# Kernel optimization log

Hardware: AMD Instinct MI355X
Metric: run time of the kernel (lower is better)

The kernel has to match this reference:

```python
import jax, jax.numpy as jnp
import numpy as np

B, C, H, W = 4, 192, 56, 56


def setup_inputs() -> dict:
    key = jax.random.key(0)
    k1, k2, k3 = jax.random.split(key, 3)
    x = jax.random.normal(k1, (B, C, H, W), dtype=jnp.float32)
    conv_w = jax.random.normal(k2, (C, 2 * C), dtype=jnp.float32) * (1.0 / np.sqrt(2 * C))
    conv_b = jax.random.normal(k3, (C,), dtype=jnp.float32) * 0.01
    bn_gamma = jnp.ones((C,), dtype=jnp.float32)
    bn_beta = jnp.zeros((C,), dtype=jnp.float32)
    bn_mean = jnp.zeros((C,), dtype=jnp.float32)
    bn_var = jnp.ones((C,), dtype=jnp.float32)
    return {"x": x, "conv_w": conv_w, "conv_b": conv_b, "bn_gamma": bn_gamma,
            "bn_beta": bn_beta, "bn_mean": bn_mean, "bn_var": bn_var, "K": 4}


def reference(x, conv_w, conv_b, bn_gamma, bn_beta, bn_mean, bn_var, K):
    b, c, h, w = x.shape
    shifts_h = list(range(0, h, K))          # rolls along H
    shifts_w = list(range(K, w, K))          # rolls along W
    n = len(shifts_h) + len(shifts_w)
    scale = n ** (-0.5)
    # (B, n, C, H, W): all circularly shifted copies (static shift set)
    rolled = jnp.stack([jnp.roll(x, i, axis=2) for i in shifts_h] +
                       [jnp.roll(x, j, axis=3) for j in shifts_w], axis=1)
    # scores: tanh(scale * x * x_rolled), summed over channels -> (B, n, 1, H, W)
    scores = jnp.tanh(rolled * x[:, None] * scale).sum(axis=2, keepdims=True)
    weights = jax.nn.softmax(scores, axis=1)
    out = (rolled * weights).sum(axis=1)     # (B, C, H, W)
    cat = jnp.concatenate([x, out], axis=1)  # (B, 2C, H, W)
    # 1x1 conv as GEMM over channels
    y = jnp.einsum('bchw,oc->bohw', cat, conv_w) + conv_b[None, :, None, None]
    # BatchNorm2d in eval mode (running stats)
    eps = 1e-5
    inv = bn_gamma / jnp.sqrt(bn_var + eps)
    y = (y - bn_mean[None, :, None, None]) * inv[None, :, None, None] + bn_beta[None, :, None, None]
    return jax.nn.gelu(y, approximate=False)
```

## Files before the change

### kernel.cpp

```cpp
#include <hip/hip_runtime.h>
#include <hip/hip_bf16.h>
#include <math.h>

#define BB 4
#define CC 192
#define HH 56
#define WW 56
#define HWW 3136

typedef __attribute__((ext_vector_type(8))) short short8;
typedef __attribute__((ext_vector_type(4))) float f32x4;

__device__ __forceinline__ unsigned short f2b(float f) {
    __hip_bfloat16 h = __float2bfloat16(f);
    return __builtin_bit_cast(unsigned short, h);
}
__device__ __forceinline__ float b2f(unsigned short u) {
    unsigned int x = ((unsigned int)u) << 16;
    return __builtin_bit_cast(float, x);
}

__global__ __launch_bounds__(256) void k_pre(const float* __restrict__ x,
                                             const float* __restrict__ cw,
                                             unsigned short* __restrict__ xth,
                                             unsigned short* __restrict__ xtl,
                                             unsigned short* __restrict__ cwh,
                                             unsigned short* __restrict__ cwl) {
    int tid = threadIdx.x, bid = blockIdx.x;
    if (bid < 2352) {
        __shared__ float tile[32][33];
        int b = bid / 588, rem = bid % 588;
        int by = rem / 98, bx = rem % 98;
        int tx = tid & 31, ty = tid >> 5;
        int p0 = bx * 32, c0 = by * 32;
#pragma unroll
        for (int i = 0; i < 4; i++) {
            int c = c0 + ty + 8 * i;
            tile[ty + 8 * i][tx] = x[(b * CC + c) * HWW + p0 + tx];
        }
        __syncthreads();
#pragma unroll
        for (int i = 0; i < 4; i++) {
            int p = p0 + ty + 8 * i;
            float v = tile[tx][ty + 8 * i];
            unsigned short hi = f2b(v);
            size_t o = (size_t)(b * HWW + p) * CC + c0 + tx;
            xth[o] = hi;
            xtl[o] = f2b(v - b2f(hi));
        }
    } else {
        int i = (bid - 2352) * 256 + tid;
        if (i < 384 * 192) {
            int n = i / 192, k = i % 192;
            float v = (n < 192) ? cw[n * 384 + k] : cw[(n - 192) * 384 + 192 + k];
            unsigned short hi = f2b(v);
            cwh[i] = hi;
            cwl[i] = f2b(v - b2f(hi));
        }
    }
}

__global__ __launch_bounds__(256) void k_mid(const unsigned short* __restrict__ xth,
                                             const unsigned short* __restrict__ xtl,
                                             const unsigned short* __restrict__ cwh,
                                             const unsigned short* __restrict__ cwl,
                                             float* __restrict__ sp,
                                             float* __restrict__ u,
                                             float* __restrict__ z) {
    __shared__ __align__(16) char smem[36864];
    int tid = threadIdx.x, bid = blockIdx.x;

    if (bid < 1792) {
        float* Xs = (float*)smem;
        const float K2 = 0.38490017945975050f;
        bool isH = bid < 896;
        int lid = isH ? bid : bid - 896;
        int half = lid & 1;
        int rp = (lid >> 1) & 1;
        int cb2 = lid >> 2;
        int b = cb2 / 56, l0 = cb2 % 56;
        int r0 = rp * 2;

        const unsigned short* srch = xth + (size_t)(b * HWW) * CC + half * 96;
        const unsigned short* srcl = xtl + (size_t)(b * HWW) * CC + half * 96;
        for (int idx = tid; idx < 28 * 12; idx += 256) {
            int t2 = idx / 12, cq = idx % 12;
            int pi = (r0 + t2 / 14) + 4 * (t2 % 14);
            int pix = isH ? (pi * WW + l0) : (l0 * WW + pi);
            short8 h8 = *(const short8*)(srch + (size_t)pix * CC + cq * 8);
            short8 l8 = *(const short8*)(srcl + (size_t)pix * CC + cq * 8);
            float o[8];
#pragma unroll
            for (int e = 0; e < 8; e++)
                o[e] = b2f((unsigned short)h8[e]) + b2f((unsigned short)l8[e]);
            *(float4*)&Xs[t2 * 100 + cq * 8] = *(float4*)&o[0];
            *(float4*)&Xs[t2 * 100 + cq * 8 + 4] = *(float4*)&o[4];
        }
        __syncthreads();

        int perCls = isH ? 105 : 91;
        if (tid < 2 * perCls) {
            int cls = tid / perCls, p = tid % perCls;
            int a, bb;
            if (isH) {
                a = (int)((sqrtf((float)(8 * p + 1)) - 1.0f) * 0.5f);
                bb = p - (a * (a + 1)) / 2;
            } else {
                int ap = (int)((sqrtf((float)(8 * p + 1)) - 1.0f) * 0.5f);
                bb = p - (ap * (ap + 1)) / 2;
                a = ap + 1;
            }
            const float* pA = &Xs[(cls * 14 + a) * 100];
            const float* pB = &Xs[(cls * 14 + bb) * 100];
            float s0 = 0.f, s1 = 0.f, s2 = 0.f, s3 = 0.f;
#pragma unroll
            for (int q = 0; q < 24; q++) {
                float4 av = *(const float4*)(pA + q * 4);
                float4 bv = *(const float4*)(pB + q * 4);
                s0 += __builtin_amdgcn_rcpf(__expf(av.x * bv.x * K2) + 1.0f);
                s1 += __builtin_amdgcn_rcpf(__expf(av.y * bv.y * K2) + 1.0f);
                s2 += __builtin_amdgcn_rcpf(__expf(av.z * bv.z * K2) + 1.0f);
                s3 += __builtin_amdgcn_rcpf(__expf(av.w * bv.w * K2) + 1.0f);
            }
            float s = 96.0f - 2.0f * (s0 + s1 + s2 + s3);
            int r = r0 + cls;
            size_t base = (size_t)(half * BB + b) * HWW;
            if (isH) {
                int i1 = a - bb;
                int h1 = r + 4 * a, h2 = r + 4 * bb;
                sp[(base + h1 * WW + l0) * 32 + i1] = s;
                if (a != bb) sp[(base + h2 * WW + l0) * 32 + (14 - i1)] = s;
            } else {
                int d = a - bb;
                int w1 = r + 4 * a, w2 = r + 4 * bb;
                sp[(base + l0 * WW + w1) * 32 + 14 + (d - 1)] = s;
                sp[(base + l0 * WW + w2) * 32 + 14 + (13 - d)] = s;
            }
        }
        return;
    }

    {
        unsigned short* Ah = (unsigned short*)smem;
        unsigned short* Al = Ah + 64 * 72;
        unsigned short* Bh = Ah + 2 * 64 * 72;
        unsigned short* Bl = Ah + 3 * 64 * 72;
        float* Ds = (float*)smem;
        int vb = bid - 1792;
        int bm = (vb % 196) * 64, bn = (vb / 196) * 64;
        int lane = tid & 63, wv = tid >> 6;

        f32x4 acc[4] = {{0,0,0,0},{0,0,0,0},{0,0,0,0},{0,0,0,0}};

        for (int kc = 0; kc < 3; kc++) {
#pragma unroll
            for (int r2 = 0; r2 < 2; r2++) {
                int idx = tid + r2 * 256;
                int m = idx >> 3, kq = idx & 7;
                size_t ao = (size_t)(bm + m) * CC + kc * 64 + kq * 8;
                *(short8*)&Ah[m * 72 + kq * 8] = *(const short8*)(xth + ao);
                *(short8*)&Al[m * 72 + kq * 8] = *(const short8*)(xtl + ao);
                size_t bo = (size_t)(bn + m) * 192 + kc * 64 + kq * 8;
                *(short8*)&Bh[m * 72 + kq * 8] = *(const short8*)(cwh + bo);
                *(short8*)&Bl[m * 72 + kq * 8] = *(const short8*)(cwl + bo);
            }
            __syncthreads();
            int n0 = wv * 16;
            int k8 = lane >> 4;
            int col = lane & 15;
#pragma unroll
            for (int ks = 0; ks < 64; ks += 32) {
                int koff = ks + k8 * 8;
                short8 bfh = *(const short8*)&Bh[(n0 + col) * 72 + koff];
                short8 bfl = *(const short8*)&Bl[(n0 + col) * 72 + koff];
#pragma unroll
                for (int fm = 0; fm < 4; fm++) {
                    short8 afh = *(const short8*)&Ah[(fm * 16 + col) * 72 + koff];
                    short8 afl = *(const short8*)&Al[(fm * 16 + col) * 72 + koff];
                    acc[fm] = __builtin_amdgcn_mfma_f32_16x16x32_bf16(afh, bfh, acc[fm], 0, 0, 0);
                    acc[fm] = __builtin_amdgcn_mfma_f32_16x16x32_bf16(afl, bfh, acc[fm], 0, 0, 0);
                    acc[fm] = __builtin_amdgcn_mfma_f32_16x16x32_bf16(afh, bfl, acc[fm], 0, 0, 0);
                }
            }
            __syncthreads();
        }
        {
            int col = lane & 15, rowq = lane >> 4;
#pragma unroll
            for (int fm = 0; fm < 4; fm++)
#pragma unroll
                for (int rg = 0; rg < 4; rg++)
                    Ds[(fm * 16 + rowq * 4 + rg) * 68 + wv * 16 + col] = acc[fm][rg];
        }
        __syncthreads();
        {
            int c4 = tid & 15, m0 = tid >> 4;
            int cg = bn + c4 * 4;
            float* dst = (cg < 192) ? u : z;
            int cc = (cg < 192) ? cg : cg - 192;
#pragma unroll
            for (int p = 0; p < 4; p++) {
                int m = m0 + p * 16;
                float4 v = *(float4*)&Ds[m * 68 + c4 * 4];
                *(float4*)&dst[(size_t)(bm + m) * CC + cc] = v;
            }
        }
    }
}

__global__ __launch_bounds__(448) void k_tail(const float* __restrict__ u,
                                              const float* __restrict__ z,
                                              const float* __restrict__ sp,
                                              const float* __restrict__ cb,
                                              const float* __restrict__ gma,
                                              const float* __restrict__ bta,
                                              const float* __restrict__ mea,
                                              const float* __restrict__ var,
                                              float* __restrict__ y) {
    __shared__ float Zs[14 * 56 * 8];
    int tid = threadIdx.x, bid = blockIdx.x;
    int th = bid & 1;
    int t1 = bid >> 1;
    int cc = t1 % 24;
    int t2 = t1 / 24;
    int r = t2 & 3;
    int b = t2 >> 2;
    int w = tid >> 3, c = tid & 7;
    int cg = cc * 8 + c;

#pragma unroll
    for (int it = 0; it < 2; it++) {
        int idx = tid + it * 448;
        if (idx < 784) {
            int t = idx / 56, ww = idx - t * 56;
            const float* s = z + ((size_t)(b * HWW + (r + 4 * t) * WW + ww)) * CC + cc * 8;
            float4 v0 = *(const float4*)s;
            float4 v1 = *(const float4*)(s + 4);
            float* d = &Zs[(t * 56 + ww) * 8];
            *(float4*)d = v0;
            *(float4*)(d + 4) = v1;
        }
    }
    __syncthreads();

    float zc[14];
#pragma unroll
    for (int m = 0; m < 14; m++) {
        int t0 = m + th * 7;
        if (t0 >= 14) t0 -= 14;
        zc[m] = Zs[(t0 * 56 + w) * 8 + c];
    }

    float bias = cb[cg];
    float ginv = gma[cg] * rsqrtf(var[cg] + 1e-5f);
    float bt = bta[cg];
    float me = mea[cg];

    int hbase = r + 4 * (th * 7);
    float acc0[7];
#pragma unroll
    for (int tt = 0; tt < 7; tt++) {
        int pix = (hbase + 4 * tt) * WW + w;
        acc0[tt] = u[((size_t)(b * HWW + pix)) * CC + cg];
    }

#pragma unroll
    for (int tt = 0; tt < 7; tt++) {
        int t = th * 7 + tt;
        int pix = (hbase + 4 * tt) * WW + w;
        size_t gp = (size_t)b * HWW + pix;

        const float4* p0 = (const float4*)&sp[gp * 32];
        const float4* p1 = (const float4*)&sp[((size_t)(4 * HWW) + gp) * 32];
        float sc[28];
#pragma unroll
        for (int j = 0; j < 7; j++) {
            float4 a4 = p0[j], v4 = p1[j];
            sc[4 * j + 0] = a4.x + v4.x; sc[4 * j + 1] = a4.y + v4.y;
            sc[4 * j + 2] = a4.z + v4.z; sc[4 * j + 3] = a4.w + v4.w;
        }
        float mx = -1e30f;
#pragma unroll
        for (int s = 0; s < 27; s++) mx = fmaxf(mx, sc[s]);
        float sum = 0.f;
#pragma unroll
        for (int s = 0; s < 27; s++) { sc[s] = __expf(sc[s] - mx); sum += sc[s]; }
        float inv = __builtin_amdgcn_rcpf(sum);

        float accw = 0.f;
#pragma unroll
        for (int i = 0; i < 14; i++)
            accw += sc[i] * zc[(tt - i + 14) % 14];
#pragma unroll
        for (int j = 1; j <= 13; j++) {
            int wj = w - 4 * j;
            if (wj < 0) wj += 56;
            accw += sc[13 + j] * Zs[(t * 56 + wj) * 8 + c];
        }
        float a = acc0[tt] + accw * inv;

        float v = (a + bias - me) * ginv + bt;
        v = 0.5f * v * (1.0f + erff(v * 0.70710678118654752f));
        y[((size_t)(b * CC + cg)) * HWW + pix] = v;
    }
}

extern "C" void kernel_launch(void* const* d_in, const int* in_sizes, int n_in,
                              void* d_out, int out_size, void* d_ws, size_t ws_size,
                              hipStream_t stream) {
    const float* x   = (const float*)d_in[0];
    const float* cw  = (const float*)d_in[1];
    const float* cb  = (const float*)d_in[2];
    const float* gma = (const float*)d_in[3];
    const float* bta = (const float*)d_in[4];
    const float* mea = (const float*)d_in[5];
    const float* var = (const float*)d_in[6];
    float* out = (float*)d_out;

    float* ws = (float*)d_ws;
    float*          sp  = ws;
    float*          u   = ws + 802816;
    float*          z   = ws + 3211264;
    unsigned short* xth = (unsigned short*)(ws + 5619712);
    unsigned short* xtl = (unsigned short*)(ws + 6823936);
    unsigned short* cwh = (unsigned short*)(ws + 8028160);
    unsigned short* cwl = (unsigned short*)(ws + 8065024);

    k_pre<<<2640, 256, 0, stream>>>(x, cw, xth, xtl, cwh, cwl);
    k_mid<<<2968, 256, 0, stream>>>(xth, xtl, cwh, cwl, sp, u, z);
    k_tail<<<768, 448, 0, stream>>>(u, z, sp, cb, gma, bta, mea, var, out);
}
```

Baseline: 135.2 us.

## Precompute softmax weights once per pixel in a separate fp16 kernel

Before, each of the 24 channel-group blocks in k_tail recomputed the 27-way softmax for every pixel from the fp32 partial scores. A new k_soft kernel now computes normalized weights once per pixel and stores them as fp16. k_tail stages those weights into shared memory and uses them directly, which removes redundant exp/max work and shrinks score reads. The cost is an extra launch, an extra workspace buffer, and fp16 rounding of the weights.

```diff
diff --git a/kernel.cpp b/kernel.cpp
--- a/kernel.cpp
+++ b/kernel.cpp
@@ -1,5 +1,6 @@
 #include <hip/hip_runtime.h>
 #include <hip/hip_bf16.h>
+#include <hip/hip_fp16.h>
 #include <math.h>
 
 #define BB 4
@@ -18,6 +19,13 @@
 __device__ __forceinline__ float b2f(unsigned short u) {
     unsigned int x = ((unsigned int)u) << 16;
     return __builtin_bit_cast(float, x);
+}
+__device__ __forceinline__ unsigned short f2h(float f) {
+    __half h = __float2half_rn(f);
+    return __builtin_bit_cast(unsigned short, h);
+}
+__device__ __forceinline__ float2 h2f2(unsigned int u) {
+    return __half22float2(__builtin_bit_cast(__half2, u));
 }
 
 __global__ __launch_bounds__(256) void k_pre(const float* __restrict__ x,
@@ -208,16 +216,48 @@
     }
 }
 
-__global__ __launch_bounds__(448) void k_tail(const float* __restrict__ u,
-                                              const float* __restrict__ z,
-                                              const float* __restrict__ sp,
-                                              const float* __restrict__ cb,
-                                              const float* __restrict__ gma,
-                                              const float* __restrict__ bta,
-                                              const float* __restrict__ mea,
-                                              const float* __restrict__ var,
-                                              float* __restrict__ y) {
+__global__ __launch_bounds__(256) void k_soft(const float* __restrict__ sp,
+                                              unsigned short* __restrict__ wn16) {
+    int gp = blockIdx.x * 256 + threadIdx.x;
+    const float4* p0 = (const float4*)&sp[(size_t)gp * 32];
+    const float4* p1 = (const float4*)&sp[((size_t)(4 * HWW) + gp) * 32];
+    float sc[28];
+#pragma unroll
+    for (int j = 0; j < 7; j++) {
+        float4 a = p0[j], v = p1[j];
+        sc[4 * j + 0] = a.x + v.x; sc[4 * j + 1] = a.y + v.y;
+        sc[4 * j + 2] = a.z + v.z; sc[4 * j + 3] = a.w + v.w;
+    }
+    float mx = -1e30f;
+#pragma unroll
+    for (int s = 0; s < 27; s++) mx = fmaxf(mx, sc[s]);
+    float sum = 0.f;
+#pragma unroll
+    for (int s = 0; s < 27; s++) { sc[s] = __expf(sc[s] - mx); sum += sc[s]; }
+    float inv = __builtin_amdgcn_rcpf(sum);
+
+    unsigned short hw[32];
+#pragma unroll
+    for (int s = 0; s < 27; s++) hw[s] = f2h(sc[s] * inv);
+#pragma unroll
+    for (int s = 27; s < 32; s++) hw[s] = 0;
+    unsigned short* dst = wn16 + (size_t)gp * 32;
+#pragma unroll
+    for (int q = 0; q < 4; q++)
+        *(short8*)(dst + q * 8) = *(short8*)&hw[q * 8];
+}
+
+__global__ __launch_bounds__(448, 1) void k_tail(const float* __restrict__ u,
+                                                 const float* __restrict__ z,
+                                                 const unsigned short* __restrict__ wn16,
+                                                 const float* __restrict__ cb,
+                                                 const float* __restrict__ gma,
+                                                 const float* __restrict__ bta,
+                                                 const float* __restrict__ mea,
+                                                 const float* __restrict__ var,
+                                                 float* __restrict__ y) {
     __shared__ float Zs[14 * 56 * 8];
+    __shared__ unsigned short W16[7 * 56 * 36];
     int tid = threadIdx.x, bid = blockIdx.x;
     int th = bid & 1;
     int t1 = bid >> 1;
@@ -227,6 +267,7 @@
     int b = t2 >> 2;
     int w = tid >> 3, c = tid & 7;
     int cg = cc * 8 + c;
+    int hbase = r + 4 * (th * 7);
 
 #pragma unroll
     for (int it = 0; it < 2; it++) {
@@ -241,6 +282,14 @@
             *(float4*)(d + 4) = v1;
         }
     }
+    for (int i = tid; i < 392 * 4; i += 448) {
+        int pl = i >> 2, q = i & 3;
+        int tq = pl / 56, ww = pl - tq * 56;
+        int row = hbase + 4 * tq;
+        size_t gsrc = ((size_t)(b * HWW + row * WW + ww)) * 32 + q * 8;
+        short8 v = *(const short8*)(wn16 + gsrc);
+        *(short8*)&W16[(tq * 56 + ww) * 36 + q * 8] = v;
+    }
     __syncthreads();
 
     float zc[14];
@@ -256,7 +305,6 @@
     float bt = bta[cg];
     float me = mea[cg];
 
-    int hbase = r + 4 * (th * 7);
     float acc0[7];
 #pragma unroll
     for (int tt = 0; tt < 7; tt++) {
@@ -268,36 +316,24 @@
     for (int tt = 0; tt < 7; tt++) {
         int t = th * 7 + tt;
         int pix = (hbase + 4 * tt) * WW + w;
-        size_t gp = (size_t)b * HWW + pix;
-
-        const float4* p0 = (const float4*)&sp[gp * 32];
-        const float4* p1 = (const float4*)&sp[((size_t)(4 * HWW) + gp) * 32];
-        float sc[28];
-#pragma unroll
-        for (int j = 0; j < 7; j++) {
-            float4 a4 = p0[j], v4 = p1[j];
-            sc[4 * j + 0] = a4.x + v4.x; sc[4 * j + 1] = a4.y + v4.y;
-            sc[4 * j + 2] = a4.z + v4.z; sc[4 * j + 3] = a4.w + v4.w;
-        }
-        float mx = -1e30f;
-#pragma unroll
-        for (int s = 0; s < 27; s++) mx = fmaxf(mx, sc[s]);
-        float sum = 0.f;
-#pragma unroll
-        for (int s = 0; s < 27; s++) { sc[s] = __expf(sc[s] - mx); sum += sc[s]; }
-        float inv = __builtin_amdgcn_rcpf(sum);
-
-        float accw = 0.f;
-#pragma unroll
-        for (int i = 0; i < 14; i++)
-            accw += sc[i] * zc[(tt - i + 14) % 14];
-#pragma unroll
-        for (int j = 1; j <= 13; j++) {
-            int wj = w - 4 * j;
-            if (wj < 0) wj += 56;
-            accw += sc[13 + j] * Zs[(t * 56 + wj) * 8 + c];
-        }
-        float a = acc0[tt] + accw * inv;
+        int pb = (tt * 56 + w) * 36;
+        float a = acc0[tt];
+
+#pragma unroll
+        for (int p = 0; p < 7; p++) {
+            float2 f2 = h2f2(*(const unsigned int*)&W16[pb + 2 * p]);
+            a += f2.x * zc[(tt - 2 * p + 28) % 14];
+            a += f2.y * zc[(tt - 2 * p - 1 + 28) % 14];
+        }
+#pragma unroll
+        for (int p = 7; p < 14; p++) {
+            float2 f2 = h2f2(*(const unsigned int*)&W16[pb + 2 * p]);
+            int j0 = 2 * p - 13, j1 = 2 * p - 12;
+            int wj0 = w - 4 * j0; if (wj0 < 0) wj0 += 56;
+            int wj1 = w - 4 * j1; if (wj1 < 0) wj1 += 56;
+            a += f2.x * Zs[(t * 56 + wj0) * 8 + c];
+            a += f2.y * Zs[(t * 56 + wj1) * 8 + c];
+        }
 
         float v = (a + bias - me) * ginv + bt;
         v = 0.5f * v * (1.0f + erff(v * 0.70710678118654752f));
@@ -318,15 +354,17 @@
     float* out = (float*)d_out;
 
     float* ws = (float*)d_ws;
-    float*          sp  = ws;
-    float*          u   = ws + 802816;
-    float*          z   = ws + 3211264;
-    unsigned short* xth = (unsigned short*)(ws + 5619712);
-    unsigned short* xtl = (unsigned short*)(ws + 6823936);
-    unsigned short* cwh = (unsigned short*)(ws + 8028160);
-    unsigned short* cwl = (unsigned short*)(ws + 8065024);
+    float*          sp   = ws;
+    float*          u    = ws + 802816;
+    float*          z    = ws + 3211264;
+    unsigned short* xth  = (unsigned short*)(ws + 5619712);
+    unsigned short* xtl  = (unsigned short*)(ws + 6823936);
+    unsigned short* cwh  = (unsigned short*)(ws + 8028160);
+    unsigned short* cwl  = (unsigned short*)(ws + 8065024);
+    unsigned short* wn16 = (unsigned short*)(ws + 8101888);
 
     k_pre<<<2640, 256, 0, stream>>>(x, cw, xth, xtl, cwh, cwl);
     k_mid<<<2968, 256, 0, stream>>>(xth, xtl, cwh, cwl, sp, u, z);
-    k_tail<<<768, 448, 0, stream>>>(u, z, sp, cb, gma, bta, mea, var, out);
-}
+    k_soft<<<49, 256, 0, stream>>>(sp, wn16);
+    k_tail<<<768, 448, 0, stream>>>(u, z, wn16, cb, gma, bta, mea, var, out);
+}
```

Result: faster. 126.5 us (-6.4%).
